# Performance work log

Hardware: AMD Instinct MI355X
Metric: run time of the kernel (lower is better)

The kernel has to match this reference:

```python
import jax, jax.numpy as jnp
import numpy as np

BS, QLEN, DIM, NHEADS, SEG = 2, 2048, 640, 8, 5
C = DIM // SEG * (SEG - 1)  # 512, channels kept after aggregator
AGG = DIM // SEG            # 128, aggregated channel slice


def setup_inputs() -> dict:
    key = jax.random.key(0)
    ks = jax.random.split(key, 12)
    s = 0.02
    return {
        "Q": jax.random.normal(ks[0], (BS, QLEN, DIM), jnp.float32),
        # Linear weights stored [in, out] so y = x @ W + b
        "W_Q": jax.random.normal(ks[1], (DIM, DIM), jnp.float32) * s,
        "b_Q": jnp.zeros((DIM,), jnp.float32),
        "W_K": jax.random.normal(ks[2], (DIM, DIM), jnp.float32) * s,
        "b_K": jnp.zeros((DIM,), jnp.float32),
        "W_V": jax.random.normal(ks[3], (DIM, DIM), jnp.float32) * s,
        "b_V": jnp.zeros((DIM,), jnp.float32),
        "W_pos": jax.random.uniform(ks[4], (QLEN, C), jnp.float32, -0.02, 0.02),
        "W_agg": jax.random.normal(ks[5], (AGG, AGG), jnp.float32) * s,
        "b_agg": jnp.zeros((AGG,), jnp.float32),
        "W_out": jax.random.normal(ks[6], (DIM, DIM), jnp.float32) * s,
        "b_out": jnp.zeros((DIM,), jnp.float32),
    }


def reference(Q, W_Q, b_Q, W_K, b_K, W_V, b_V, W_pos, W_agg, b_agg, W_out, b_out):
    bs, L, dim = Q.shape
    hd = C // NHEADS  # per-head dim after aggregation (64)
    # self-attention: K = V = Q
    q = Q @ W_Q + b_Q
    k = Q @ W_K + b_K
    v = Q @ W_V + b_V
    qkv = jnp.stack([q, k, v])  # [3, bs, L, dim]
    # Aggregator: keep first 4/5 channels per branch, aggregate last 1/5 across q/k/v
    x_main = qkv[..., :C]                                   # [3, bs, L, C]
    x_agg0 = jax.nn.gelu(qkv[..., C:].mean(0) @ W_agg + b_agg)  # [bs, L, AGG]
    # pos embedding add (dropout is identity at eval)
    q_s = (x_main[0] + W_pos).reshape(bs, L, NHEADS, hd).transpose(0, 2, 1, 3)  # [bs,H,L,hd]
    k_s = (x_main[1] + W_pos).reshape(bs, L, NHEADS, hd).transpose(0, 2, 3, 1)  # [bs,H,hd,L]
    v_s = (x_main[2] + W_pos).reshape(bs, L, NHEADS, hd).transpose(0, 2, 1, 3)  # [bs,H,L,hd]
    scale = (DIM // NHEADS) ** -0.5  # note: uses dim//n_heads (80), not post-agg head dim
    scores = jnp.einsum("bhqd,bhdk->bhqk", q_s, k_s) * scale  # [bs,H,L,L]
    attn = jax.nn.softmax(scores, axis=-1)
    out = jnp.einsum("bhqk,bhkd->bhqd", attn, v_s)             # [bs,H,L,hd]
    out = out.transpose(0, 2, 1, 3).reshape(bs, L, C)
    out = jnp.concatenate([out, x_agg0], axis=-1) @ W_out + b_out  # [bs,L,dim]
    return out, attn
```

## Files before the change

kernel.cpp:

```cpp
#include <hip/hip_runtime.h>
#include <cstdint>
#include <cstddef>

#define BSZ   2
#define QL    2048
#define DIMN  640
#define NH    8
#define CMAIN 512
#define AGGD  128
#define MROWS 4096
#define SCALE_QK 0.11180339887498948f
#define C2EXP (SCALE_QK * 1.4426950408889634f)

typedef __bf16 bf16;
typedef __bf16 bf16x8 __attribute__((ext_vector_type(8)));
typedef __bf16 bf16x4v __attribute__((ext_vector_type(4)));
typedef float  f32x4  __attribute__((ext_vector_type(4)));

typedef __attribute__((address_space(1))) const uint32_t GU32;
typedef __attribute__((address_space(3))) uint32_t LU32;
#define GLL(g, l) __builtin_amdgcn_global_load_lds((GU32*)(g), (LU32*)(l), 16, 0, 0)

#define EXP2F(x) __builtin_amdgcn_exp2f(x)
#define LOG2F(x) __builtin_amdgcn_logf(x)

static __device__ __forceinline__ f32x4 mfma16(bf16x8 a, bf16x8 b, f32x4 c) {
    return __builtin_amdgcn_mfma_f32_16x16x32_bf16(a, b, c, 0, 0, 0);
}

static __device__ __forceinline__ void waitbar() {
    asm volatile("s_waitcnt vmcnt(0)" ::: "memory");
    __builtin_amdgcn_s_barrier();
    asm volatile("" ::: "memory");
}

template<int ROWB>
static __device__ __forceinline__ bf16x8 ldsfragR(const bf16* base, int row, int kbyte) {
    return *(const bf16x8*)((const char*)base + row * ROWB + (kbyte ^ ((row & 7) << 4)));
}

template<int NCH, int ROWB, int NT>
static __device__ __forceinline__ void stage_rowsN(bf16* ldsbuf, const char* gbase,
                                                   int strideB, int tid) {
    const int lane = tid & 63;
    const int wbase = tid - lane;
    #pragma unroll
    for (int i = 0; i < NCH / NT; ++i) {
        int c = i * NT + tid;
        int r = c / (ROWB / 16);
        int kb = ((c % (ROWB / 16)) * 16) ^ ((r & 7) << 4);
        GLL(gbase + (size_t)r * strideB + kb,
            (char*)ldsbuf + (size_t)(i * NT + wbase) * 16);
    }
}

template<int MI>
static __device__ __forceinline__ void gemm_main(
    const bf16* __restrict__ A, const bf16* __restrict__ BT,
    int m0, int n0, bf16* lds, f32x4 acc[MI][4])
{
    const int tid = threadIdx.x;
    const int w = tid >> 6, lane = tid & 63;
    const int lr = lane & 15, lg = lane >> 4;
    const int wm = (w >> 1) * (MI * 16), wn = (w & 1) * 64;
    constexpr int ASZ = MI * 2048;
    constexpr int BUF = ASZ + 8192;

    stage_rowsN<MI * 256, 128, 256>(lds,   (const char*)(A + (size_t)m0 * 640), 1280, tid);
    stage_rowsN<1024, 128, 256>(lds + ASZ, (const char*)(BT + (size_t)n0 * 640), 1280, tid);
    int cur = 0;
    #pragma unroll 1
    for (int ch = 0; ch < 10; ++ch) {
        waitbar();
        if (ch < 9) {
            int kk = (ch + 1) * 64;
            bf16* nb = lds + (cur ^ 1) * BUF;
            stage_rowsN<MI * 256, 128, 256>(nb,   (const char*)(A + (size_t)m0 * 640 + kk), 1280, tid);
            stage_rowsN<1024, 128, 256>(nb + ASZ, (const char*)(BT + (size_t)n0 * 640 + kk), 1280, tid);
        }
        const bf16* cA = lds + cur * BUF;
        const bf16* cB = cA + ASZ;
        #pragma unroll
        for (int ks = 0; ks < 2; ++ks) {
            bf16x8 a[MI], b[4];
            #pragma unroll
            for (int i = 0; i < MI; ++i) a[i] = ldsfragR<128>(cA, wm + i * 16 + lr, ks * 64 + lg * 16);
            #pragma unroll
            for (int i = 0; i < 4; ++i)  b[i] = ldsfragR<128>(cB, wn + i * 16 + lr, ks * 64 + lg * 16);
            #pragma unroll
            for (int mi = 0; mi < MI; ++mi)
                #pragma unroll
                for (int ni = 0; ni < 4; ++ni)
                    acc[mi][ni] = mfma16(a[mi], b[ni], acc[mi][ni]);
        }
        cur ^= 1;
    }
}

__global__ void __launch_bounds__(256) k_split_q(const float* __restrict__ Q,
                                                 bf16* __restrict__ Qbf) {
    int i = blockIdx.x * 256 + threadIdx.x;
    float4 v = ((const float4*)Q)[i];
    bf16x4v hv;
    hv[0] = (bf16)v.x; hv[1] = (bf16)v.y; hv[2] = (bf16)v.z; hv[3] = (bf16)v.w;
    *(bf16x4v*)(Qbf + (size_t)i * 4) = hv;
}

__global__ void __launch_bounds__(256) k_prep_w(
    const float* __restrict__ WQ, const float* __restrict__ WK,
    const float* __restrict__ WV, const float* __restrict__ WO,
    bf16* __restrict__ BTqkv, bf16* __restrict__ BTout)
{
    __shared__ float tl[64][65];
    const int ty = blockIdx.x / 10, tx = blockIdx.x % 10;
    const int wsel = blockIdx.y;
    const float* W = (wsel == 0) ? WQ : (wsel == 1) ? WK : (wsel == 2) ? WV : WO;
    const int tid = threadIdx.x;
    const int rr = tid >> 4;
    const int cc = (tid & 15) * 4;
    #pragma unroll
    for (int i = 0; i < 4; ++i) {
        int k = tx * 64 + rr + i * 16;
        float4 v = *(const float4*)(W + (size_t)k * 640 + ty * 64 + cc);
        tl[cc + 0][rr + i * 16] = v.x;
        tl[cc + 1][rr + i * 16] = v.y;
        tl[cc + 2][rr + i * 16] = v.z;
        tl[cc + 3][rr + i * 16] = v.w;
    }
    __syncthreads();
    bf16* dst; int nbase;
    if (wsel < 3) { dst = BTqkv; nbase = wsel * 640 + ty * 64; }
    else          { dst = BTout; nbase = ty * 64; }
    const int nl0 = tid >> 4;
    const int kl = (tid & 15) * 4;
    #pragma unroll
    for (int i = 0; i < 4; ++i) {
        int nl = nl0 + i * 16;
        bf16x4v hv;
        #pragma unroll
        for (int j = 0; j < 4; ++j) hv[j] = (bf16)tl[nl][kl + j];
        *(bf16x4v*)(dst + (size_t)(nbase + nl) * 640 + tx * 64 + kl) = hv;
    }
}

__global__ void __launch_bounds__(256) k_gemm_qkv(
    const bf16* __restrict__ Qbf, const bf16* __restrict__ BT,
    const float* __restrict__ bQ, const float* __restrict__ bK, const float* __restrict__ bV,
    const float* __restrict__ Wpos,
    bf16* __restrict__ qsbuf, bf16* __restrict__ vsT, float* __restrict__ aggbuf)
{
    __shared__ __align__(16) bf16 lds[2 * (8192 + 8192)];
    const int m0 = blockIdx.x * 128, n0 = blockIdx.y * 128;
    f32x4 acc[4][4];
    {
        f32x4 z = {0.f, 0.f, 0.f, 0.f};
        #pragma unroll
        for (int mi = 0; mi < 4; ++mi)
            #pragma unroll
            for (int ni = 0; ni < 4; ++ni) acc[mi][ni] = z;
    }
    gemm_main<4>(Qbf, BT, m0, n0, lds, acc);

    const int tid = threadIdx.x, w = tid >> 6, lane = tid & 63;
    const int lr = lane & 15, lg = lane >> 4;
    const int wm = (w >> 1) * 64, wn = (w & 1) * 64;
    const int p = n0 / 640;
    const float* bias = (p == 0) ? bQ : (p == 1) ? bK : bV;

    #pragma unroll
    for (int mi = 0; mi < 4; ++mi)
        #pragma unroll
        for (int ni = 0; ni < 4; ++ni) {
            int n = n0 + wn + ni * 16 + lr;
            int c = n - p * 640;
            int rbase = m0 + wm + mi * 16 + lg * 4;
            float bval = bias[c];
            if (c < 512) {
                int hh = c >> 6, d = c & 63;
                #pragma unroll
                for (int r = 0; r < 4; ++r) {
                    int rg = rbase + r;
                    int bb = rg >> 11, l = rg & 2047;
                    float v = acc[mi][ni][r] + bval + Wpos[(size_t)l * 512 + c];
                    if (p < 2)
                        qsbuf[(((size_t)(p * 2 + bb) * 8 + hh) * 2048 + l) * 64 + d] = (bf16)v;
                    else
                        vsT[(((size_t)(bb * 8 + hh)) * 64 + d) * 2048 + l] = (bf16)v;
                }
            } else {
                int j = c - 512;
                #pragma unroll
                for (int r = 0; r < 4; ++r) {
                    int rg = rbase + r;
                    aggbuf[((size_t)p * MROWS + rg) * AGGD + j] = acc[mi][ni][r] + bval;
                }
            }
        }
}

__global__ void __launch_bounds__(256) k_agg(const float* __restrict__ aggbuf,
                                             const float* __restrict__ Wagg, const float* __restrict__ bagg,
                                             bf16* __restrict__ xcat)
{
    __shared__ float wl[128 * 128];
    __shared__ float xl[32 * 128];
    const int tid = threadIdx.x;
    const int r0 = blockIdx.x * 32;
    for (int i = tid; i < 128 * 128; i += 256) wl[i] = Wagg[i];
    for (int i = tid; i < 32 * 128; i += 256) {
        int row = i >> 7, j = i & 127;
        size_t rg = r0 + row;
        float s = aggbuf[rg * AGGD + j]
                + aggbuf[((size_t)MROWS + rg) * AGGD + j]
                + aggbuf[((size_t)2 * MROWS + rg) * AGGD + j];
        xl[i] = s * (1.0f / 3.0f);
    }
    __syncthreads();
    const int row = tid >> 3;
    const int jo0 = (tid & 7) * 16;
    float acc[16];
    #pragma unroll
    for (int jj = 0; jj < 16; ++jj) acc[jj] = 0.f;
    for (int j = 0; j < 128; ++j) {
        float xv = xl[row * 128 + j];
        const float* wr = &wl[j * 128 + jo0];
        #pragma unroll
        for (int jj = 0; jj < 16; ++jj) acc[jj] = fmaf(xv, wr[jj], acc[jj]);
    }
    size_t rg = r0 + row;
    #pragma unroll
    for (int jj = 0; jj < 16; ++jj) {
        float t = acc[jj] + bagg[jo0 + jj];
        float g = 0.5f * t * (1.0f + tanhf(0.7978845608028654f * (t + 0.044715f * t * t * t)));
        xcat[rg * 640 + 512 + jo0 + jj] = (bf16)g;
    }
}

__global__ void __launch_bounds__(512) k_attn(const bf16* __restrict__ qsbuf, const bf16* __restrict__ vsT,
                                              float* __restrict__ gattn,
                                              bf16* __restrict__ xcat)
{
    __shared__ __align__(16) bf16 smem[2][16384];
    __shared__ __align__(16) bf16 p_lds[8][16 * 128];

    const int bh = blockIdx.y;
    const int b = bh >> 3, h = bh & 7;
    const int q0 = blockIdx.x * 128;
    const int tid = threadIdx.x, w = tid >> 6, lane = tid & 63;
    const int lr = lane & 15, lg = lane >> 4;

    const bf16* qbase = qsbuf + (size_t)(b * 8 + h) * (2048 * 64);
    const bf16* kbase = qsbuf + (size_t)((2 + b) * 8 + h) * (2048 * 64);
    const bf16* vtb   = vsT + (size_t)(b * 8 + h) * (64 * 2048);

    bf16x8 aq[2];
    {
        const bf16* qp = qbase + (size_t)(q0 + w * 16 + lr) * 64 + lg * 8;
        aq[0] = *(const bf16x8*)(qp);
        aq[1] = *(const bf16x8*)(qp + 32);
    }

    float lsum = 0.f;
    stage_rowsN<1024, 128, 512>(smem[0], (const char*)kbase, 128, tid);
    int cur = 0;
    #pragma unroll 1
    for (int kt = 0; kt < 16; ++kt) {
        waitbar();
        if (kt < 15)
            stage_rowsN<1024, 128, 512>(smem[cur ^ 1], (const char*)kbase + (size_t)(kt + 1) * 16384, 128, tid);
        __builtin_amdgcn_sched_barrier(0);
        const bf16* kb = smem[cur];
        f32x4 s[8];
        {
            f32x4 z = {0.f, 0.f, 0.f, 0.f};
            #pragma unroll
            for (int ni = 0; ni < 8; ++ni) s[ni] = z;
        }
        #pragma unroll
        for (int ks = 0; ks < 2; ++ks)
            #pragma unroll
            for (int ni = 0; ni < 8; ++ni)
                s[ni] = mfma16(ldsfragR<128>(kb, ni * 16 + lr, ks * 64 + lg * 16), aq[ks], s[ni]);
        #pragma unroll
        for (int ni = 0; ni < 8; ++ni)
            #pragma unroll
            for (int r = 0; r < 4; ++r)
                lsum += EXP2F(s[ni][r] * C2EXP);
        cur ^= 1;
    }
    lsum += __shfl_xor(lsum, 16);
    lsum += __shfl_xor(lsum, 32);
    const float l2i = -LOG2F(lsum);

    f32x4 o[4];
    {
        f32x4 z = {0.f, 0.f, 0.f, 0.f};
        #pragma unroll
        for (int ni = 0; ni < 4; ++ni) o[ni] = z;
    }
    float* attnrow = gattn + (size_t)bh * 2048 * 2048 + (size_t)(q0 + w * 16 + lr) * 2048;

    stage_rowsN<1024, 128, 512>(smem[0],        (const char*)kbase, 128, tid);
    stage_rowsN<1024, 256, 512>(smem[0] + 8192, (const char*)vtb, 4096, tid);
    cur = 0;
    #pragma unroll 1
    for (int kt = 0; kt < 16; ++kt) {
        if (kt == 0) asm volatile("s_waitcnt vmcnt(0)" ::: "memory");
        else         asm volatile("s_waitcnt vmcnt(8)" ::: "memory");
        __builtin_amdgcn_s_barrier();
        asm volatile("" ::: "memory");
        if (kt < 15) {
            stage_rowsN<1024, 128, 512>(smem[cur ^ 1],        (const char*)kbase + (size_t)(kt + 1) * 16384, 128, tid);
            stage_rowsN<1024, 256, 512>(smem[cur ^ 1] + 8192, (const char*)vtb + (size_t)(kt + 1) * 256, 4096, tid);
        }
        __builtin_amdgcn_sched_barrier(0);
        const bf16* kb = smem[cur];
        const bf16* vb = smem[cur] + 8192;
        f32x4 s[8];
        {
            f32x4 z = {0.f, 0.f, 0.f, 0.f};
            #pragma unroll
            for (int ni = 0; ni < 8; ++ni) s[ni] = z;
        }
        #pragma unroll
        for (int ks = 0; ks < 2; ++ks)
            #pragma unroll
            for (int ni = 0; ni < 8; ++ni)
                s[ni] = mfma16(ldsfragR<128>(kb, ni * 16 + lr, ks * 64 + lg * 16), aq[ks], s[ni]);
        bf16* pl = &p_lds[w][0];
        float* arow = attnrow + kt * 128;
        #pragma unroll
        for (int ni = 0; ni < 8; ++ni) {
            f32x4 p;
            #pragma unroll
            for (int r = 0; r < 4; ++r) p[r] = EXP2F(fmaf(s[ni][r], C2EXP, l2i));
            *(f32x4*)(arow + ni * 16 + lg * 4) = p;
            bf16x4v pb;
            #pragma unroll
            for (int r = 0; r < 4; ++r) pb[r] = (bf16)p[r];
            *(bf16x4v*)((char*)pl + lr * 256 + ((ni * 32 + lg * 8) ^ ((lr & 7) << 4))) = pb;
        }
        #pragma unroll
        for (int ks = 0; ks < 4; ++ks) {
            bf16x8 pa = ldsfragR<256>(pl, lr, ks * 64 + lg * 16);
            #pragma unroll
            for (int ni = 0; ni < 4; ++ni)
                o[ni] = mfma16(pa, ldsfragR<256>(vb, ni * 16 + lr, ks * 64 + lg * 16), o[ni]);
        }
        cur ^= 1;
    }

    #pragma unroll
    for (int ni = 0; ni < 4; ++ni) {
        #pragma unroll
        for (int r = 0; r < 4; ++r) {
            int qr = q0 + w * 16 + lg * 4 + r;
            size_t rg = (size_t)b * 2048 + qr;
            int c = h * 64 + ni * 16 + lr;
            xcat[rg * 640 + c] = (bf16)o[ni][r];
        }
    }
}

__global__ void __launch_bounds__(256) k_gemm_out(
    const bf16* __restrict__ X, const bf16* __restrict__ BT,
    const float* __restrict__ bout, float* __restrict__ out0)
{
    __shared__ __align__(16) bf16 lds[2 * (4096 + 8192)];
    const int m0 = blockIdx.x * 64, n0 = blockIdx.y * 128;
    f32x4 acc[2][4];
    {
        f32x4 z = {0.f, 0.f, 0.f, 0.f};
        #pragma unroll
        for (int mi = 0; mi < 2; ++mi)
            #pragma unroll
            for (int ni = 0; ni < 4; ++ni) acc[mi][ni] = z;
    }
    gemm_main<2>(X, BT, m0, n0, lds, acc);

    const int tid = threadIdx.x, w = tid >> 6, lane = tid & 63;
    const int lr = lane & 15, lg = lane >> 4;
    const int wm = (w >> 1) * 32, wn = (w & 1) * 64;
    #pragma unroll
    for (int mi = 0; mi < 2; ++mi)
        #pragma unroll
        for (int ni = 0; ni < 4; ++ni) {
            int n = n0 + wn + ni * 16 + lr;
            float bv = bout[n];
            #pragma unroll
            for (int r = 0; r < 4; ++r) {
                int rg = m0 + wm + mi * 16 + lg * 4 + r;
                out0[(size_t)rg * 640 + n] = acc[mi][ni][r] + bv;
            }
        }
}

extern "C" void kernel_launch(void* const* d_in, const int* in_sizes, int n_in,
                              void* d_out, int out_size, void* d_ws, size_t ws_size,
                              hipStream_t stream)
{
    (void)in_sizes; (void)n_in; (void)out_size; (void)ws_size;
    const float* Q    = (const float*)d_in[0];
    const float* WQ   = (const float*)d_in[1];
    const float* bQ   = (const float*)d_in[2];
    const float* WK   = (const float*)d_in[3];
    const float* bK   = (const float*)d_in[4];
    const float* WV   = (const float*)d_in[5];
    const float* bV   = (const float*)d_in[6];
    const float* Wpos = (const float*)d_in[7];
    const float* Wagg = (const float*)d_in[8];
    const float* bagg = (const float*)d_in[9];
    const float* WO   = (const float*)d_in[10];
    const float* bout = (const float*)d_in[11];

    float* out0  = (float*)d_out;
    float* gattn = out0 + (size_t)MROWS * DIMN;

    char* ws = (char*)d_ws;
    bf16* Qbf    = (bf16*)(ws);                 ws += (size_t)MROWS * DIMN * 2;
    bf16* BTqkv  = (bf16*)(ws);                 ws += (size_t)1920 * 640 * 2;
    bf16* BTout  = (bf16*)(ws);                 ws += (size_t)640 * 640 * 2;
    bf16* qsbuf  = (bf16*)(ws);                 ws += (size_t)4 * 8 * 2048 * 64 * 2;
    bf16* vsT    = (bf16*)(ws);                 ws += (size_t)16 * 64 * 2048 * 2;
    float* aggbuf= (float*)(ws);                ws += (size_t)3 * MROWS * AGGD * 4;
    bf16* xcat   = (bf16*)(ws);                 ws += (size_t)MROWS * DIMN * 2;

    k_split_q<<<dim3(2560), dim3(256), 0, stream>>>(Q, Qbf);
    k_prep_w<<<dim3(100, 4), dim3(256), 0, stream>>>(WQ, WK, WV, WO, BTqkv, BTout);
    k_gemm_qkv<<<dim3(32, 15), dim3(256), 0, stream>>>(Qbf, BTqkv,
                                                       bQ, bK, bV, Wpos, qsbuf, vsT, aggbuf);
    k_agg<<<dim3(128), dim3(256), 0, stream>>>(aggbuf, Wagg, bagg, xcat);
    k_attn<<<dim3(16, 16), dim3(512), 0, stream>>>(qsbuf, vsT, gattn, xcat);
    k_gemm_out<<<dim3(64, 5), dim3(256), 0, stream>>>(xcat, BTout, bout, out0);
}
```

Before: 163.2 us.

## Shrink attention blocks to 64 queries and triple-buffer K/V staging

The attention kernel now runs 256-thread blocks over 64 query rows, which doubles the grid to 512 blocks. The K/V tiles are halved to 64 keys in the second pass. Staging moves from double buffering to a three-stage ring with deeper vmcnt waits, so loads run two tiles ahead of compute. The aim is higher occupancy with less LDS per block, and better latency hiding for the large attention-matrix write. In exchange, each loop iteration has more barriers and K is reloaded by twice as many blocks.

```diff
diff --git a/kernel.cpp b/kernel.cpp
--- a/kernel.cpp
+++ b/kernel.cpp
@@ -236,16 +236,16 @@
     }
 }
 
-__global__ void __launch_bounds__(512) k_attn(const bf16* __restrict__ qsbuf, const bf16* __restrict__ vsT,
+__global__ void __launch_bounds__(256) k_attn(const bf16* __restrict__ qsbuf, const bf16* __restrict__ vsT,
                                               float* __restrict__ gattn,
                                               bf16* __restrict__ xcat)
 {
-    __shared__ __align__(16) bf16 smem[2][16384];
-    __shared__ __align__(16) bf16 p_lds[8][16 * 128];
+    __shared__ __align__(16) bf16 smem[3][8192];
+    __shared__ __align__(16) bf16 p_lds[4][1024];
 
     const int bh = blockIdx.y;
     const int b = bh >> 3, h = bh & 7;
-    const int q0 = blockIdx.x * 128;
+    const int q0 = blockIdx.x * 64;
     const int tid = threadIdx.x, w = tid >> 6, lane = tid & 63;
     const int lr = lane & 15, lg = lane >> 4;
 
@@ -261,15 +261,19 @@
     }
 
     float lsum = 0.f;
-    stage_rowsN<1024, 128, 512>(smem[0], (const char*)kbase, 128, tid);
-    int cur = 0;
+    stage_rowsN<1024, 128, 256>(smem[0], (const char*)kbase, 128, tid);
+    stage_rowsN<1024, 128, 256>(smem[1], (const char*)kbase + 16384, 128, tid);
     #pragma unroll 1
     for (int kt = 0; kt < 16; ++kt) {
-        waitbar();
-        if (kt < 15)
-            stage_rowsN<1024, 128, 512>(smem[cur ^ 1], (const char*)kbase + (size_t)(kt + 1) * 16384, 128, tid);
+        if (kt < 15) asm volatile("s_waitcnt vmcnt(4)" ::: "memory");
+        else         asm volatile("s_waitcnt vmcnt(0)" ::: "memory");
+        __builtin_amdgcn_s_barrier();
+        asm volatile("" ::: "memory");
+        if (kt < 14)
+            stage_rowsN<1024, 128, 256>(smem[(kt + 2) % 3],
+                                        (const char*)kbase + (size_t)(kt + 2) * 16384, 128, tid);
         __builtin_amdgcn_sched_barrier(0);
-        const bf16* kb = smem[cur];
+        const bf16* kb = smem[kt % 3];
         f32x4 s[8];
         {
             f32x4 z = {0.f, 0.f, 0.f, 0.f};
@@ -286,8 +290,8 @@
             #pragma unroll
             for (int r = 0; r < 4; ++r)
                 lsum += EXP2F(s[ni][r] * C2EXP);
-        cur ^= 1;
-    }
+    }
+    __syncthreads();
     lsum += __shfl_xor(lsum, 16);
     lsum += __shfl_xor(lsum, 32);
     const float l2i = -LOG2F(lsum);
@@ -300,37 +304,41 @@
     }
     float* attnrow = gattn + (size_t)bh * 2048 * 2048 + (size_t)(q0 + w * 16 + lr) * 2048;
 
-    stage_rowsN<1024, 128, 512>(smem[0],        (const char*)kbase, 128, tid);
-    stage_rowsN<1024, 256, 512>(smem[0] + 8192, (const char*)vtb, 4096, tid);
-    cur = 0;
+    stage_rowsN<512, 128, 256>(smem[0],        (const char*)kbase, 128, tid);
+    stage_rowsN<512, 128, 256>(smem[0] + 4096, (const char*)vtb, 4096, tid);
+    stage_rowsN<512, 128, 256>(smem[1],        (const char*)kbase + 8192, 128, tid);
+    stage_rowsN<512, 128, 256>(smem[1] + 4096, (const char*)vtb + 128, 4096, tid);
     #pragma unroll 1
-    for (int kt = 0; kt < 16; ++kt) {
-        if (kt == 0) asm volatile("s_waitcnt vmcnt(0)" ::: "memory");
-        else         asm volatile("s_waitcnt vmcnt(8)" ::: "memory");
+    for (int kt = 0; kt < 32; ++kt) {
+        if (kt == 0)       asm volatile("s_waitcnt vmcnt(4)" ::: "memory");
+        else if (kt == 1)  asm volatile("s_waitcnt vmcnt(8)" ::: "memory");
+        else if (kt == 31) asm volatile("s_waitcnt vmcnt(8)" ::: "memory");
+        else               asm volatile("s_waitcnt vmcnt(12)" ::: "memory");
         __builtin_amdgcn_s_barrier();
         asm volatile("" ::: "memory");
-        if (kt < 15) {
-            stage_rowsN<1024, 128, 512>(smem[cur ^ 1],        (const char*)kbase + (size_t)(kt + 1) * 16384, 128, tid);
-            stage_rowsN<1024, 256, 512>(smem[cur ^ 1] + 8192, (const char*)vtb + (size_t)(kt + 1) * 256, 4096, tid);
+        if (kt < 30) {
+            bf16* nb = smem[(kt + 2) % 3];
+            stage_rowsN<512, 128, 256>(nb,        (const char*)kbase + (size_t)(kt + 2) * 8192, 128, tid);
+            stage_rowsN<512, 128, 256>(nb + 4096, (const char*)vtb + (size_t)(kt + 2) * 128, 4096, tid);
         }
         __builtin_amdgcn_sched_barrier(0);
-        const bf16* kb = smem[cur];
-        const bf16* vb = smem[cur] + 8192;
-        f32x4 s[8];
+        const bf16* kb = smem[kt % 3];
+        const bf16* vb = kb + 4096;
+        f32x4 s[4];
         {
             f32x4 z = {0.f, 0.f, 0.f, 0.f};
             #pragma unroll
-            for (int ni = 0; ni < 8; ++ni) s[ni] = z;
+            for (int ni = 0; ni < 4; ++ni) s[ni] = z;
         }
         #pragma unroll
         for (int ks = 0; ks < 2; ++ks)
             #pragma unroll
-            for (int ni = 0; ni < 8; ++ni)
+            for (int ni = 0; ni < 4; ++ni)
                 s[ni] = mfma16(ldsfragR<128>(kb, ni * 16 + lr, ks * 64 + lg * 16), aq[ks], s[ni]);
         bf16* pl = &p_lds[w][0];
-        float* arow = attnrow + kt * 128;
-        #pragma unroll
-        for (int ni = 0; ni < 8; ++ni) {
+        float* arow = attnrow + kt * 64;
+        #pragma unroll
+        for (int ni = 0; ni < 4; ++ni) {
             f32x4 p;
             #pragma unroll
             for (int r = 0; r < 4; ++r) p[r] = EXP2F(fmaf(s[ni][r], C2EXP, l2i));
@@ -338,16 +346,15 @@
             bf16x4v pb;
             #pragma unroll
             for (int r = 0; r < 4; ++r) pb[r] = (bf16)p[r];
-            *(bf16x4v*)((char*)pl + lr * 256 + ((ni * 32 + lg * 8) ^ ((lr & 7) << 4))) = pb;
-        }
-        #pragma unroll
-        for (int ks = 0; ks < 4; ++ks) {
-            bf16x8 pa = ldsfragR<256>(pl, lr, ks * 64 + lg * 16);
+            *(bf16x4v*)((char*)pl + lr * 128 + ((ni * 32 + lg * 8) ^ ((lr & 7) << 4))) = pb;
+        }
+        #pragma unroll
+        for (int ks = 0; ks < 2; ++ks) {
+            bf16x8 pa = ldsfragR<128>(pl, lr, ks * 64 + lg * 16);
             #pragma unroll
             for (int ni = 0; ni < 4; ++ni)
-                o[ni] = mfma16(pa, ldsfragR<256>(vb, ni * 16 + lr, ks * 64 + lg * 16), o[ni]);
-        }
-        cur ^= 1;
+                o[ni] = mfma16(pa, ldsfragR<128>(vb, ni * 16 + lr, ks * 64 + lg * 16), o[ni]);
+        }
     }
 
     #pragma unroll
@@ -430,6 +437,6 @@
     k_gemm_qkv<<<dim3(32, 15), dim3(256), 0, stream>>>(Qbf, BTqkv,
                                                        bQ, bK, bV, Wpos, qsbuf, vsT, aggbuf);
     k_agg<<<dim3(128), dim3(256), 0, stream>>>(aggbuf, Wagg, bagg, xcat);
-    k_attn<<<dim3(16, 16), dim3(512), 0, stream>>>(qsbuf, vsT, gattn, xcat);
+    k_attn<<<dim3(32, 16), dim3(256), 0, stream>>>(qsbuf, vsT, gattn, xcat);
     k_gemm_out<<<dim3(64, 5), dim3(256), 0, stream>>>(xcat, BTout, bout, out0);
 }
```

New measurement: 161.4 us. About the same (-1.1%).
